# Optimization experiments

Hardware: AMD Instinct MI355X
Metric: run time of the kernel (lower is better)

Reference implementation:

```python
import jax, jax.numpy as jnp
import numpy as np
from functools import partial

EPS = 1e-5
SCALE = 2
NUM_BLOCKS = 2


def _layernorm(x, g, b):
    mu = jnp.mean(x, axis=-1, keepdims=True)
    var = jnp.var(x, axis=-1, keepdims=True)
    return (x - mu) * jax.lax.rsqrt(var + EPS) * g + b


def _rwkv(tokens, td, Wk, Wv, Wr, Wo, ln_g, ln_b):
    # tokens: (B, N, C)
    x = _layernorm(tokens, ln_g, ln_b)
    k = jnp.einsum('bnc,oc->bno', x, Wk)
    v = jnp.einsum('bnc,oc->bno', x, Wv)
    r = jax.nn.sigmoid(jnp.einsum('bnc,oc->bno', x, Wr))
    decay = jnp.exp(-jax.nn.relu(td))  # (C,)

    def step(state, inp):
        kt, vt, rt = inp  # each (B, C)
        state = state * decay + kt
        return state, rt * (state + vt)

    B, N, C = tokens.shape
    init = jnp.zeros((B, C), dtype=tokens.dtype)
    # scan over token axis
    _, yT = jax.lax.scan(step, init, (k.transpose(1, 0, 2), v.transpose(1, 0, 2), r.transpose(1, 0, 2)))
    y = yT.transpose(1, 0, 2)  # (B, N, C)
    return jnp.einsum('bnc,oc->bno', y, Wo)


def reference(x, global_state, cond_gw, cond_gb, cond_bw, cond_bb,
              td, Wk, Wv, Wr, Wo, ln_g, ln_b, gp_w, gp_b, bp_w, bp_b):
    B, C, H, W = x.shape
    Hp, Wp = H * SCALE, W * SCALE
    # bilinear upsample, half-pixel centers == torch align_corners=False
    x_up = jax.image.resize(x, (B, C, Hp, Wp), method='bilinear')
    tokens = x_up.reshape(B, C, Hp * Wp).transpose(0, 2, 1)  # (B, N, C)
    # semantic conditioning (FiLM from global state)
    gamma = (global_state @ cond_gw.T + cond_gb)[:, None, :]
    beta = (global_state @ cond_bw.T + cond_bb)[:, None, :]
    tokens = tokens * (1.0 + gamma) + beta

    out = x_up
    cur = tokens
    for i in range(NUM_BLOCKS):
        if i > 0:
            cur = out.reshape(B, C, Hp * Wp).transpose(0, 2, 1)
        t = _rwkv(cur, td[i], Wk[i], Wv[i], Wr[i], Wo[i], ln_g[i], ln_b[i])
        g = jnp.einsum('bnc,oc->bno', t, gp_w[i]) + gp_b[i]
        bt = jnp.einsum('bnc,oc->bno', t, bp_w[i]) + bp_b[i]
        g = g.transpose(0, 2, 1).reshape(B, C, Hp, Wp)
        bt = bt.transpose(0, 2, 1).reshape(B, C, Hp, Wp)
        out = out * (1.0 + jnp.tanh(g)) + bt
    return out


def setup_inputs() -> dict:
    key = jax.random.key(0)
    ks = jax.random.split(key, 16)
    B, C, H, W = 8, 128, 64, 64
    w_scale = 0.02
    inp = {
        'x': jax.random.normal(ks[0], (B, C, H, W), jnp.float32),
        'global_state': jax.random.normal(ks[1], (B, C), jnp.float32),
        'cond_gw': jax.random.normal(ks[2], (C, C), jnp.float32) * w_scale,
        'cond_gb': jnp.zeros((C,), jnp.float32),
        'cond_bw': jax.random.normal(ks[3], (C, C), jnp.float32) * w_scale,
        'cond_bb': jnp.zeros((C,), jnp.float32),
        'td': jax.random.uniform(ks[4], (NUM_BLOCKS, C), jnp.float32),
        'Wk': jax.random.normal(ks[5], (NUM_BLOCKS, C, C), jnp.float32) * w_scale,
        'Wv': jax.random.normal(ks[6], (NUM_BLOCKS, C, C), jnp.float32) * w_scale,
        'Wr': jax.random.normal(ks[7], (NUM_BLOCKS, C, C), jnp.float32) * w_scale,
        'Wo': jax.random.normal(ks[8], (NUM_BLOCKS, C, C), jnp.float32) * w_scale,
        'ln_g': jnp.ones((NUM_BLOCKS, C), jnp.float32),
        'ln_b': jnp.zeros((NUM_BLOCKS, C), jnp.float32),
        'gp_w': jax.random.normal(ks[9], (NUM_BLOCKS, C, C), jnp.float32) * w_scale,
        'gp_b': jnp.zeros((NUM_BLOCKS, C), jnp.float32),
        'bp_w': jax.random.normal(ks[10], (NUM_BLOCKS, C, C), jnp.float32) * w_scale,
        'bp_b': jnp.zeros((NUM_BLOCKS, C), jnp.float32),
    }
    return inp
```

## Files before the change

kernel.cpp:

```cpp
#include <hip/hip_runtime.h>
#include <hip/hip_bf16.h>

#define BB 8
#define CC 128
#define NN 16384
#define MM (BB * NN)
#define NCH 128
#define CLN 128

typedef __attribute__((ext_vector_type(8))) short short8;
typedef __attribute__((ext_vector_type(4))) float floatx4;
typedef unsigned short u16;
typedef unsigned int u32;

__device__ __forceinline__ float bf2f(u16 h) {
  u32 u = ((u32)h) << 16;
  return __builtin_bit_cast(float, u);
}
__device__ __forceinline__ u16 f2bf(float f) {
  u32 u = __builtin_bit_cast(u32, f);
  u32 r = u + 0x7FFFu + ((u >> 16) & 1u);
  return (u16)(r >> 16);
}

__global__ void film_kernel(const float* __restrict__ gs, const float* __restrict__ gw,
                            const float* __restrict__ gb, const float* __restrict__ bw,
                            const float* __restrict__ bb, float* __restrict__ gamma,
                            float* __restrict__ beta) {
  int idx = blockIdx.x * 256 + threadIdx.x;
  int b = idx >> 7, c = idx & 127;
  float sg = 0.f, sb = 0.f;
  for (int j = 0; j < 128; ++j) {
    float g = gs[b * 128 + j];
    sg += g * gw[c * 128 + j];
    sb += g * bw[c * 128 + j];
  }
  gamma[idx] = sg + gb[c];
  beta[idx] = sb + bb[c];
}

__global__ void convert_kernel(const float* __restrict__ Wk, const float* __restrict__ Wv,
                               const float* __restrict__ Wr, const float* __restrict__ Wo,
                               const float* __restrict__ gp, const float* __restrict__ bp,
                               u16* __restrict__ dst) {
  int idx = blockIdx.x * 256 + threadIdx.x;
  int which = idx >> 15;
  int off = idx & 32767;
  const float* s;
  switch (which) {
    case 0: s = Wk; break; case 1: s = Wv; break; case 2: s = Wr; break;
    case 3: s = Wo; break; case 4: s = gp; break; default: s = bp; break;
  }
  dst[idx] = f2bf(s[off]);
}

template <int UPS>
__global__ __launch_bounds__(256) void prep_kernel(
    const float* __restrict__ src, const float* __restrict__ gamma,
    const float* __restrict__ beta, const float* __restrict__ lng,
    const float* __restrict__ lnb, float* __restrict__ outp, u16* __restrict__ xn) {
  __shared__ float tile[64][129];
  __shared__ float smu[64], srs[64];
  int bidx = blockIdx.x;
  int half = bidx & 1;
  int ho = (bidx >> 1) & 127;
  int b = bidx >> 8;
  int wo0 = half * 64;
  int tid = threadIdx.x;
  int tk = tid & 63;
  int wo = wo0 + tk;
  int c0 = tid >> 6;
  int j0 = 0, j1 = 0, i0 = 0, i1 = 0;
  float wy0 = 0.f, wy1 = 0.f, wx0 = 0.f, wx1 = 0.f;
  if (UPS) {
    int jj = ho >> 1;
    if ((ho & 1) == 0) { j0 = jj > 0 ? jj - 1 : 0; j1 = jj; wy0 = 0.25f; wy1 = 0.75f; }
    else               { j0 = jj; j1 = jj < 63 ? jj + 1 : 63; wy0 = 0.75f; wy1 = 0.25f; }
    int ii = wo >> 1;
    if ((wo & 1) == 0) { i0 = ii > 0 ? ii - 1 : 0; i1 = ii; wx0 = 0.25f; wx1 = 0.75f; }
    else               { i0 = ii; i1 = ii < 63 ? ii + 1 : 63; wx0 = 0.75f; wx1 = 0.25f; }
  }
  for (int it = 0; it < 32; ++it) {
    int c = it * 4 + c0;
    float v;
    if (UPS) {
      const float* xp = src + ((size_t)(b * 128 + c)) * 4096;
      v = wy0 * (wx0 * xp[j0 * 64 + i0] + wx1 * xp[j0 * 64 + i1]) +
          wy1 * (wx0 * xp[j1 * 64 + i0] + wx1 * xp[j1 * 64 + i1]);
      outp[((size_t)(b * 128 + c)) * 16384 + ho * 128 + wo] = v;
      v = v * (1.f + gamma[b * 128 + c]) + beta[b * 128 + c];
    } else {
      v = src[((size_t)(b * 128 + c)) * 16384 + ho * 128 + wo];
    }
    tile[tk][c] = v;
  }
  __syncthreads();
  {
    int token = tid >> 2, q = tid & 3;
    float s = 0.f, s2 = 0.f;
    for (int j = 0; j < 32; ++j) { float v = tile[token][q * 32 + j]; s += v; s2 += v * v; }
    s += __shfl_xor(s, 1); s2 += __shfl_xor(s2, 1);
    s += __shfl_xor(s, 2); s2 += __shfl_xor(s2, 2);
    if (q == 0) {
      float mu = s * 0.0078125f;
      float var = s2 * 0.0078125f - mu * mu;
      smu[token] = mu;
      srs[token] = rsqrtf(var + 1e-5f);
    }
  }
  __syncthreads();
  size_t base = ((size_t)b * 16384 + ho * 128 + wo0) * 128;
  for (int it = 0; it < 32; ++it) {
    int idx = it * 256 + tid;
    int token = idx >> 7, c = idx & 127;
    float v = (tile[token][c] - smu[token]) * srs[token] * lng[c] + lnb[c];
    xn[base + idx] = f2bf(v);
  }
}

__global__ __launch_bounds__(256, 2) void gemm_y_kernel(
    const u16* __restrict__ A, const u16* __restrict__ Wv_, const u16* __restrict__ Wr_,
    const u16* __restrict__ Wk_, const float* __restrict__ td,
    u16* __restrict__ outY, u16* __restrict__ outRD, float* __restrict__ Sbuf) {
  __shared__ u16 Alds[128 * 128];
  __shared__ u16 Wlds[128 * 128];
  __shared__ float SWT[512];
  int tid = threadIdx.x;
  int wave = tid >> 6, lane = tid & 63;
  int l15 = lane & 15, l4 = lane >> 4;
  size_t row0 = (size_t)blockIdx.x * 128;

#pragma unroll
  for (int it = 0; it < 8; ++it) {
    int idx = it * 256 + tid;
    int rr = idx >> 4, s = idx & 15;
    uint4 d = *(const uint4*)(A + (row0 + rr) * 128 + s * 8);
    *(uint4*)(&Alds[rr * 128 + ((s ^ (rr & 15)) << 3)]) = d;
  }
#pragma unroll
  for (int it = 0; it < 8; ++it) {
    int idx = it * 256 + tid;
    int rr = idx >> 4, s = idx & 15;
    uint4 d = *(const uint4*)(Wv_ + rr * 128 + s * 8);
    *(uint4*)(&Wlds[rr * 128 + ((s ^ (rr & 15)) << 3)]) = d;
  }
  float av[8], dd[8], d4a[8];
#pragma unroll
  for (int ni = 0; ni < 8; ++ni) {
    float a = fmaxf(td[ni * 16 + l15], 0.f);
    av[ni] = a;
    float d = __expf(-a);
    dd[ni] = d;
    float d2 = d * d;
    d4a[ni] = d2 * d2;
  }
  __syncthreads();

  floatx4 accv[2][8];
#pragma unroll
  for (int mi = 0; mi < 2; ++mi)
#pragma unroll
    for (int ni = 0; ni < 8; ++ni) accv[mi][ni] = (floatx4){0.f, 0.f, 0.f, 0.f};
#pragma unroll
  for (int kk = 0; kk < 4; ++kk) {
    int seg = kk * 4 + l4;
    short8 a0 = *(const short8*)(&Alds[(wave * 32 + l15) * 128 + ((seg ^ l15) << 3)]);
    short8 a1 = *(const short8*)(&Alds[(wave * 32 + 16 + l15) * 128 + ((seg ^ l15) << 3)]);
#pragma unroll
    for (int ni = 0; ni < 8; ++ni) {
      short8 bfr = *(const short8*)(&Wlds[(ni * 16 + l15) * 128 + ((seg ^ l15) << 3)]);
      accv[0][ni] = __builtin_amdgcn_mfma_f32_16x16x32_bf16(a0, bfr, accv[0][ni], 0, 0, 0);
      accv[1][ni] = __builtin_amdgcn_mfma_f32_16x16x32_bf16(a1, bfr, accv[1][ni], 0, 0, 0);
    }
  }
  __syncthreads();
#pragma unroll
  for (int it = 0; it < 8; ++it) {
    int idx = it * 256 + tid;
    int rr = idx >> 4, s = idx & 15;
    uint4 d = *(const uint4*)(Wr_ + rr * 128 + s * 8);
    *(uint4*)(&Wlds[rr * 128 + ((s ^ (rr & 15)) << 3)]) = d;
  }
  __syncthreads();
  floatx4 accr[2][8];
#pragma unroll
  for (int mi = 0; mi < 2; ++mi)
#pragma unroll
    for (int ni = 0; ni < 8; ++ni) accr[mi][ni] = (floatx4){0.f, 0.f, 0.f, 0.f};
#pragma unroll
  for (int kk = 0; kk < 4; ++kk) {
    int seg = kk * 4 + l4;
    short8 a0 = *(const short8*)(&Alds[(wave * 32 + l15) * 128 + ((seg ^ l15) << 3)]);
    short8 a1 = *(const short8*)(&Alds[(wave * 32 + 16 + l15) * 128 + ((seg ^ l15) << 3)]);
#pragma unroll
    for (int ni = 0; ni < 8; ++ni) {
      short8 bfr = *(const short8*)(&Wlds[(ni * 16 + l15) * 128 + ((seg ^ l15) << 3)]);
      accr[0][ni] = __builtin_amdgcn_mfma_f32_16x16x32_bf16(a0, bfr, accr[0][ni], 0, 0, 0);
      accr[1][ni] = __builtin_amdgcn_mfma_f32_16x16x32_bf16(a1, bfr, accr[1][ni], 0, 0, 0);
    }
  }
  u32 rvp[2][8][2], rp[2][8][2];
#pragma unroll
  for (int mi = 0; mi < 2; ++mi) {
#pragma unroll
    for (int ni = 0; ni < 8; ++ni) {
      int c = ni * 16 + l15;
      int T0 = wave * 32 + mi * 16 + l4 * 4;
      float w = __expf(-av[ni] * (float)(T0 + 1));
      float rs[4], rv[4];
#pragma unroll
      for (int j = 0; j < 4; ++j) {
        float sg = 1.f / (1.f + __expf(-accr[mi][ni][j]));
        rs[j] = sg;
        rv[j] = sg * accv[mi][ni][j];
        outRD[(row0 + T0 + j) * 128 + c] = f2bf(sg * w);
        w *= dd[ni];
      }
      rvp[mi][ni][0] = (u32)f2bf(rv[0]) | ((u32)f2bf(rv[1]) << 16);
      rvp[mi][ni][1] = (u32)f2bf(rv[2]) | ((u32)f2bf(rv[3]) << 16);
      rp[mi][ni][0] = (u32)f2bf(rs[0]) | ((u32)f2bf(rs[1]) << 16);
      rp[mi][ni][1] = (u32)f2bf(rs[2]) | ((u32)f2bf(rs[3]) << 16);
    }
  }
  __syncthreads();
#pragma unroll
  for (int it = 0; it < 8; ++it) {
    int idx = it * 256 + tid;
    int rr = idx >> 4, s = idx & 15;
    uint4 d = *(const uint4*)(Wk_ + rr * 128 + s * 8);
    *(uint4*)(&Wlds[rr * 128 + ((s ^ (rr & 15)) << 3)]) = d;
  }
  __syncthreads();
  floatx4 acck[2][8];
#pragma unroll
  for (int mi = 0; mi < 2; ++mi)
#pragma unroll
    for (int ni = 0; ni < 8; ++ni) acck[mi][ni] = (floatx4){0.f, 0.f, 0.f, 0.f};
#pragma unroll
  for (int kk = 0; kk < 4; ++kk) {
    int seg = kk * 4 + l4;
    short8 a0 = *(const short8*)(&Alds[(wave * 32 + l15) * 128 + ((seg ^ l15) << 3)]);
    short8 a1 = *(const short8*)(&Alds[(wave * 32 + 16 + l15) * 128 + ((seg ^ l15) << 3)]);
#pragma unroll
    for (int ni = 0; ni < 8; ++ni) {
      short8 bfr = *(const short8*)(&Wlds[(ni * 16 + l15) * 128 + ((seg ^ l15) << 3)]);
      acck[0][ni] = __builtin_amdgcn_mfma_f32_16x16x32_bf16(a0, bfr, acck[0][ni], 0, 0, 0);
      acck[1][ni] = __builtin_amdgcn_mfma_f32_16x16x32_bf16(a1, bfr, acck[1][ni], 0, 0, 0);
    }
  }
  float Elr[2][8];
  float B0r[8];
#pragma unroll
  for (int ni = 0; ni < 8; ++ni) {
    float d = dd[ni], d4 = d4a[ni];
    float d8 = d4 * d4, d16 = d8 * d8;
    float I[2];
#pragma unroll
    for (int mi = 0; mi < 2; ++mi) {
      float p0 = acck[mi][ni][0];
      float p1 = d * p0 + acck[mi][ni][1];
      float p2 = d * p1 + acck[mi][ni][2];
      float p3 = d * p2 + acck[mi][ni][3];
      acck[mi][ni][0] = p0; acck[mi][ni][1] = p1;
      acck[mi][ni][2] = p2; acck[mi][ni][3] = p3;
      float Iv = p3;
      float t1 = __shfl_up(Iv, 16);
      if (l4 >= 1) Iv += d4 * t1;
      float t2 = __shfl_up(Iv, 32);
      if (l4 >= 2) Iv += d8 * t2;
      float ex = __shfl_up(Iv, 16);
      Elr[mi][ni] = (l4 == 0) ? 0.f : ex;
      I[mi] = Iv;
    }
    float B0 = __shfl(I[0], 48 + l15);
    float B1 = __shfl(I[1], 48 + l15);
    B0r[ni] = B0;
    if (l4 == 0) SWT[wave * 128 + ni * 16 + l15] = B1 + d16 * B0;
  }
  __syncthreads();
  u16* YW = Wlds;
#pragma unroll
  for (int ni = 0; ni < 8; ++ni) {
    int c = ni * 16 + l15;
    float d = dd[ni], d4 = d4a[ni];
    float d8 = d4 * d4, d12 = d8 * d4, d16 = d8 * d8, d32 = d16 * d16;
    float e = 0.f;
#pragma unroll
    for (int wv = 0; wv < 3; ++wv)
      if (wv < wave) e = e * d32 + SWT[wv * 128 + c];
    float d4l = (l4 == 0) ? 1.f : ((l4 == 1) ? d4 : ((l4 == 2) ? d8 : d12));
#pragma unroll
    for (int mi = 0; mi < 2; ++mi) {
      float Emi = (mi == 0) ? e : (e * d16 + B0r[ni]);
      float Sb = Elr[mi][ni] + d4l * Emi;
      float w = d;
#pragma unroll
      for (int j = 0; j < 4; ++j) {
        float s = acck[mi][ni][j] + w * Sb;
        w *= d;
        float rvv = bf2f((u16)(rvp[mi][ni][j >> 1] >> ((j & 1) * 16)));
        float rss = bf2f((u16)(rp[mi][ni][j >> 1] >> ((j & 1) * 16)));
        float y = rvv + rss * s;
        int row = wave * 32 + mi * 16 + l4 * 4 + j;
        int colsw = c ^ (((row >> 2) & 3) << 4);
        YW[row * 128 + colsw] = f2bf(y);
      }
    }
  }
  if (tid < 128) {
    float a = fmaxf(td[tid], 0.f);
    float d32 = __expf(-32.f * a);
    float e = 0.f;
#pragma unroll
    for (int wv = 0; wv < 4; ++wv) e = e * d32 + SWT[wv * 128 + tid];
    Sbuf[(blockIdx.x & 127) * 1024 + (blockIdx.x >> 7) * 128 + tid] = e;
  }
  __syncthreads();
#pragma unroll
  for (int it = 0; it < 8; ++it) {
    int idx = it * 256 + tid;
    int row = idx >> 4, cb = (idx & 15) * 8;
    int csw = cb ^ (((row >> 2) & 3) << 4);
    uint4 dv = *(const uint4*)(&YW[row * 128 + csw]);
    *(uint4*)(outY + (row0 + row) * 128 + cb) = dv;
  }
}

__global__ __launch_bounds__(256) void scan2_kernel(const float* __restrict__ S,
                                                    const float* __restrict__ td,
                                                    float* __restrict__ init) {
  int wave = threadIdx.x >> 6, lane = threadIdx.x & 63;
  int bc = blockIdx.x * 4 + wave;
  int c = bc & 127;
  float a1 = __expf(-fmaxf(td[c], 0.f) * 128.f);
  float s0 = S[(2 * lane) * 1024 + bc];
  float s1 = S[(2 * lane + 1) * 1024 + bc];
  float s = s1 + a1 * s0;
  float a = a1 * a1;
  for (int off = 1; off < 64; off <<= 1) {
    float ss = __shfl_up(s, off);
    float aa = __shfl_up(a, off);
    if (lane >= off) { s = s + a * ss; a = a * aa; }
  }
  float e = __shfl_up(s, 1);
  if (lane == 0) e = 0.f;
  init[(2 * lane) * 1024 + bc] = e;
  init[(2 * lane + 1) * 1024 + bc] = a1 * e + s0;
}

__global__ __launch_bounds__(512, 4) void tail_kernel(
    const u16* __restrict__ yl, const u16* __restrict__ rd,
    const float* __restrict__ init,
    const u16* __restrict__ Wo, const u16* __restrict__ Wg, const u16* __restrict__ Wb,
    const float* __restrict__ gpb, const float* __restrict__ bpb,
    float* __restrict__ outp) {
  __shared__ u32 SMEM[8192];
  __shared__ float IL[128];
  u16* Y = (u16*)SMEM;
  u16* T2 = (u16*)SMEM;
  u32* MB = SMEM;

  int tid = threadIdx.x;
  int wave = tid >> 6, lane = tid & 63;
  int l15 = lane & 15, l4 = lane >> 4;
  int b = blockIdx.x >> 7;
  int chunk = blockIdx.x & 127;
  size_t ebase = ((size_t)b * 16384 + (size_t)chunk * 128) * 128;

  if (tid < 128) IL[tid] = init[chunk * 1024 + b * 128 + tid];
  __syncthreads();

#pragma unroll
  for (int it = 0; it < 4; ++it) {
    int idx = it * 512 + tid;
    int t = idx >> 4;
    int c8 = (idx & 15) * 8;
    uint4 yv = *(const uint4*)(yl + ebase + (size_t)t * 128 + c8);
    uint4 rv = *(const uint4*)(rd + ebase + (size_t)t * 128 + c8);
    u32 o[4];
    u32 yq[4] = {yv.x, yv.y, yv.z, yv.w};
    u32 rq[4] = {rv.x, rv.y, rv.z, rv.w};
#pragma unroll
    for (int q = 0; q < 4; ++q) {
      float y0 = bf2f((u16)(yq[q] & 0xffff)) + bf2f((u16)(rq[q] & 0xffff)) * IL[c8 + 2 * q];
      float y1 = bf2f((u16)(yq[q] >> 16)) + bf2f((u16)(rq[q] >> 16)) * IL[c8 + 2 * q + 1];
      o[q] = (u32)f2bf(y0) | ((u32)f2bf(y1) << 16);
    }
    uint4 ov = {o[0], o[1], o[2], o[3]};
    *(uint4*)(&Y[t * 128 + (((c8 >> 3) ^ (t & 15)) << 3)]) = ov;
  }
  __syncthreads();

  int ob = wave * 16;
  short8 wof[4];
#pragma unroll
  for (int kk = 0; kk < 4; ++kk)
    wof[kk] = *(const short8*)(Wo + (ob + l15) * 128 + kk * 32 + l4 * 8);
  floatx4 acc[8];
#pragma unroll
  for (int ni = 0; ni < 8; ++ni) acc[ni] = (floatx4){0.f, 0.f, 0.f, 0.f};
#pragma unroll
  for (int kk = 0; kk < 4; ++kk) {
    int seg = kk * 4 + l4;
#pragma unroll
    for (int ni = 0; ni < 8; ++ni) {
      short8 yf = *(const short8*)(&Y[(ni * 16 + l15) * 128 + ((seg ^ l15) << 3)]);
      acc[ni] = __builtin_amdgcn_mfma_f32_16x16x32_bf16(wof[kk], yf, acc[ni], 0, 0, 0);
    }
  }
  __syncthreads();

#pragma unroll
  for (int ni = 0; ni < 8; ++ni) {
    int tok = ni * 16 + l15;
#pragma unroll
    for (int j = 0; j < 4; j += 2) {
      int o = ob + l4 * 4 + j;
      u32 pack = (u32)f2bf(acc[ni][j]) | ((u32)f2bf(acc[ni][j + 1]) << 16);
      int pos = tok * 128 + ((((o >> 3) ^ (tok & 15)) << 3) | (o & 7));
      *(u32*)(T2 + pos) = pack;
    }
  }
  __syncthreads();

  short8 wgf[4], wbf2[4];
#pragma unroll
  for (int kk = 0; kk < 4; ++kk) {
    wgf[kk]  = *(const short8*)(Wg + (ob + l15) * 128 + kk * 32 + l4 * 8);
    wbf2[kk] = *(const short8*)(Wb + (ob + l15) * 128 + kk * 32 + l4 * 8);
  }
  floatx4 ag[8], ab[8];
#pragma unroll
  for (int ni = 0; ni < 8; ++ni) {
    ag[ni] = (floatx4){0.f, 0.f, 0.f, 0.f};
    ab[ni] = (floatx4){0.f, 0.f, 0.f, 0.f};
  }
#pragma unroll
  for (int kk = 0; kk < 4; ++kk) {
    int seg = kk * 4 + l4;
#pragma unroll
    for (int ni = 0; ni < 8; ++ni) {
      short8 tf = *(const short8*)(&T2[(ni * 16 + l15) * 128 + ((seg ^ l15) << 3)]);
      ag[ni] = __builtin_amdgcn_mfma_f32_16x16x32_bf16(wgf[kk], tf, ag[ni], 0, 0, 0);
      ab[ni] = __builtin_amdgcn_mfma_f32_16x16x32_bf16(wbf2[kk], tf, ab[ni], 0, 0, 0);
    }
  }
  __syncthreads();

#pragma unroll
  for (int h = 0; h < 2; ++h) {
    if ((wave >> 2) == h) {
      int orel0 = (wave & 3) * 16;
#pragma unroll
      for (int ni = 0; ni < 8; ++ni) {
        int tok = ni * 16 + l15;
#pragma unroll
        for (int j = 0; j < 4; ++j) {
          int orel = orel0 + l4 * 4 + j;
          int o = h * 64 + orel;
          float g = ag[ni][j] + gpb[o];
          float t1 = __expf(2.f * g);
          float m = 2.f - 2.f / (t1 + 1.f);
          float bt = ab[ni][j] + bpb[o];
          int rot = ((orel & 3) << 2) | ((orel >> 2) & 3);
          MB[orel * 128 + ((((tok >> 3) ^ rot) << 3) | (tok & 7))] =
              (u32)f2bf(m) | ((u32)f2bf(bt) << 16);
        }
      }
    }
    __syncthreads();
#pragma unroll
    for (int it = 0; it < 2; ++it) {
      int idx = it * 512 + tid;
      int orel = idx >> 4, seg = idx & 15;
      int o = h * 64 + orel;
      int rot = ((orel & 3) << 2) | ((orel >> 2) & 3);
      int sp = ((seg ^ rot) << 3);
      uint4 mb0 = *(const uint4*)(&MB[orel * 128 + sp]);
      uint4 mb1 = *(const uint4*)(&MB[orel * 128 + sp + 4]);
      float* op = outp + ((size_t)(b * 128 + o)) * 16384 + chunk * 128 + seg * 8;
      float4 o0 = *(float4*)op;
      float4 o1 = *(float4*)(op + 4);
      o0.x = o0.x * bf2f((u16)(mb0.x & 0xffff)) + bf2f((u16)(mb0.x >> 16));
      o0.y = o0.y * bf2f((u16)(mb0.y & 0xffff)) + bf2f((u16)(mb0.y >> 16));
      o0.z = o0.z * bf2f((u16)(mb0.z & 0xffff)) + bf2f((u16)(mb0.z >> 16));
      o0.w = o0.w * bf2f((u16)(mb0.w & 0xffff)) + bf2f((u16)(mb0.w >> 16));
      o1.x = o1.x * bf2f((u16)(mb1.x & 0xffff)) + bf2f((u16)(mb1.x >> 16));
      o1.y = o1.y * bf2f((u16)(mb1.y & 0xffff)) + bf2f((u16)(mb1.y >> 16));
      o1.z = o1.z * bf2f((u16)(mb1.z & 0xffff)) + bf2f((u16)(mb1.z >> 16));
      o1.w = o1.w * bf2f((u16)(mb1.w & 0xffff)) + bf2f((u16)(mb1.w >> 16));
      *(float4*)op = o0;
      *(float4*)(op + 4) = o1;
    }
    __syncthreads();
  }
}

extern "C" void kernel_launch(void* const* d_in, const int* in_sizes, int n_in,
                              void* d_out, int out_size, void* d_ws, size_t ws_size,
                              hipStream_t stream) {
  const float* x        = (const float*)d_in[0];
  const float* gs       = (const float*)d_in[1];
  const float* cond_gw  = (const float*)d_in[2];
  const float* cond_gb  = (const float*)d_in[3];
  const float* cond_bw  = (const float*)d_in[4];
  const float* cond_bb  = (const float*)d_in[5];
  const float* td       = (const float*)d_in[6];
  const float* Wk       = (const float*)d_in[7];
  const float* Wv       = (const float*)d_in[8];
  const float* Wr       = (const float*)d_in[9];
  const float* Wo       = (const float*)d_in[10];
  const float* ln_g     = (const float*)d_in[11];
  const float* ln_b     = (const float*)d_in[12];
  const float* gp_w     = (const float*)d_in[13];
  const float* gp_b     = (const float*)d_in[14];
  const float* bp_w     = (const float*)d_in[15];
  const float* bp_b     = (const float*)d_in[16];
  float* outp = (float*)d_out;

  char* w = (char*)d_ws;
  float* gamma = (float*)w; w += 4096;
  float* beta  = (float*)w; w += 4096;
  u16* wbf     = (u16*)w;   w += 6 * 2 * 16384 * sizeof(u16);
  u16* xn      = (u16*)w;   w += (size_t)MM * 128 * sizeof(u16);
  u16* ybuf    = (u16*)w;   w += (size_t)MM * 128 * sizeof(u16);
  u16* rdbuf   = (u16*)w;   w += (size_t)MM * 128 * sizeof(u16);
  float* Sbuf  = (float*)w; w += NCH * 1024 * sizeof(float);
  float* ibuf  = (float*)w; w += NCH * 1024 * sizeof(float);

  film_kernel<<<4, 256, 0, stream>>>(gs, cond_gw, cond_gb, cond_bw, cond_bb, gamma, beta);
  convert_kernel<<<768, 256, 0, stream>>>(Wk, Wv, Wr, Wo, gp_w, bp_w, wbf);

  for (int blk = 0; blk < 2; ++blk) {
    const u16* bWk = wbf + 0 * 32768 + blk * 16384;
    const u16* bWv = wbf + 1 * 32768 + blk * 16384;
    const u16* bWr = wbf + 2 * 32768 + blk * 16384;
    const u16* bWo = wbf + 3 * 32768 + blk * 16384;
    const u16* bGp = wbf + 4 * 32768 + blk * 16384;
    const u16* bBp = wbf + 5 * 32768 + blk * 16384;
    const float* tdi = td + blk * 128;

    if (blk == 0)
      prep_kernel<1><<<2048, 256, 0, stream>>>(x, gamma, beta, ln_g, ln_b, outp, xn);
    else
      prep_kernel<0><<<2048, 256, 0, stream>>>(outp, nullptr, nullptr, ln_g + 128,
                                               ln_b + 128, nullptr, xn);

    gemm_y_kernel<<<1024, 256, 0, stream>>>(xn, bWv, bWr, bWk, tdi, ybuf, rdbuf, Sbuf);
    scan2_kernel<<<256, 256, 0, stream>>>(Sbuf, tdi, ibuf);
    tail_kernel<<<1024, 512, 0, stream>>>(ybuf, rdbuf, ibuf, bWo, bGp, bBp,
                                          gp_b + blk * 128, bp_b + blk * 128, outp);
  }
}
```

Measured before the change: 268.9 us.

## Compute chunk states in separate pass to drop intermediate rd buffer

```diff
diff --git a/kernel.cpp b/kernel.cpp
--- a/kernel.cpp
+++ b/kernel.cpp
@@ -118,18 +118,16 @@
   }
 }
 
-__global__ __launch_bounds__(256, 2) void gemm_y_kernel(
-    const u16* __restrict__ A, const u16* __restrict__ Wv_, const u16* __restrict__ Wr_,
-    const u16* __restrict__ Wk_, const float* __restrict__ td,
-    u16* __restrict__ outY, u16* __restrict__ outRD, float* __restrict__ Sbuf) {
+__global__ __launch_bounds__(256) void gemm_S_kernel(
+    const u16* __restrict__ A, const u16* __restrict__ W0,
+    const float* __restrict__ td, float* __restrict__ Sbuf) {
   __shared__ u16 Alds[128 * 128];
   __shared__ u16 Wlds[128 * 128];
-  __shared__ float SWT[512];
+  __shared__ float Sred[512];
   int tid = threadIdx.x;
   int wave = tid >> 6, lane = tid & 63;
   int l15 = lane & 15, l4 = lane >> 4;
   size_t row0 = (size_t)blockIdx.x * 128;
-
 #pragma unroll
   for (int it = 0; it < 8; ++it) {
     int idx = it * 256 + tid;
@@ -141,14 +139,111 @@
   for (int it = 0; it < 8; ++it) {
     int idx = it * 256 + tid;
     int rr = idx >> 4, s = idx & 15;
+    uint4 d = *(const uint4*)(W0 + rr * 128 + s * 8);
+    *(uint4*)(&Wlds[rr * 128 + ((s ^ (rr & 15)) << 3)]) = d;
+  }
+  __syncthreads();
+  floatx4 acc[2][8];
+#pragma unroll
+  for (int mi = 0; mi < 2; ++mi)
+#pragma unroll
+    for (int ni = 0; ni < 8; ++ni) acc[mi][ni] = (floatx4){0.f, 0.f, 0.f, 0.f};
+#pragma unroll
+  for (int kk = 0; kk < 4; ++kk) {
+    int seg = kk * 4 + l4;
+    short8 a0 = *(const short8*)(&Alds[(wave * 32 + l15) * 128 + ((seg ^ l15) << 3)]);
+    short8 a1 = *(const short8*)(&Alds[(wave * 32 + 16 + l15) * 128 + ((seg ^ l15) << 3)]);
+#pragma unroll
+    for (int ni = 0; ni < 8; ++ni) {
+      short8 bfr = *(const short8*)(&Wlds[(ni * 16 + l15) * 128 + ((seg ^ l15) << 3)]);
+      acc[0][ni] = __builtin_amdgcn_mfma_f32_16x16x32_bf16(a0, bfr, acc[0][ni], 0, 0, 0);
+      acc[1][ni] = __builtin_amdgcn_mfma_f32_16x16x32_bf16(a1, bfr, acc[1][ni], 0, 0, 0);
+    }
+  }
+  int T0 = wave * 32 + l4 * 4;
+#pragma unroll
+  for (int ni = 0; ni < 8; ++ni) {
+    int c = ni * 16 + l15;
+    float a = fmaxf(td[c], 0.f);
+    float E = __expf(-a * (float)(127 - T0));
+    float r1 = __expf(a);
+    float r16 = __expf(a * 16.f);
+    float w = E, sum;
+    sum  = w * acc[0][ni][0]; w *= r1;
+    sum += w * acc[0][ni][1]; w *= r1;
+    sum += w * acc[0][ni][2]; w *= r1;
+    sum += w * acc[0][ni][3];
+    w = E * r16;
+    sum += w * acc[1][ni][0]; w *= r1;
+    sum += w * acc[1][ni][1]; w *= r1;
+    sum += w * acc[1][ni][2]; w *= r1;
+    sum += w * acc[1][ni][3];
+    sum += __shfl_xor(sum, 16);
+    sum += __shfl_xor(sum, 32);
+    if (l4 == 0) Sred[wave * 128 + c] = sum;
+  }
+  __syncthreads();
+  if (tid < 128) {
+    float s = Sred[tid] + Sred[128 + tid] + Sred[256 + tid] + Sred[384 + tid];
+    Sbuf[(blockIdx.x & 127) * 1024 + (blockIdx.x >> 7) * 128 + tid] = s;
+  }
+}
+
+__global__ __launch_bounds__(256) void scan2_kernel(const float* __restrict__ S,
+                                                    const float* __restrict__ td,
+                                                    float* __restrict__ init) {
+  int wave = threadIdx.x >> 6, lane = threadIdx.x & 63;
+  int bc = blockIdx.x * 4 + wave;
+  int c = bc & 127;
+  float a1 = __expf(-fmaxf(td[c], 0.f) * 128.f);
+  float s0 = S[(2 * lane) * 1024 + bc];
+  float s1 = S[(2 * lane + 1) * 1024 + bc];
+  float s = s1 + a1 * s0;
+  float a = a1 * a1;
+  for (int off = 1; off < 64; off <<= 1) {
+    float ss = __shfl_up(s, off);
+    float aa = __shfl_up(a, off);
+    if (lane >= off) { s = s + a * ss; a = a * aa; }
+  }
+  float e = __shfl_up(s, 1);
+  if (lane == 0) e = 0.f;
+  init[(2 * lane) * 1024 + bc] = e;
+  init[(2 * lane + 1) * 1024 + bc] = a1 * e + s0;
+}
+
+__global__ __launch_bounds__(256, 2) void gemm_y_kernel(
+    const u16* __restrict__ A, const u16* __restrict__ Wv_, const u16* __restrict__ Wr_,
+    const u16* __restrict__ Wk_, const float* __restrict__ td,
+    const float* __restrict__ init_, u16* __restrict__ outY) {
+  __shared__ u16 Alds[128 * 128];
+  __shared__ u16 Wlds[128 * 128];
+  __shared__ float SWT[512];
+  __shared__ float ILS[128];
+  int tid = threadIdx.x;
+  int wave = tid >> 6, lane = tid & 63;
+  int l15 = lane & 15, l4 = lane >> 4;
+  size_t row0 = (size_t)blockIdx.x * 128;
+  int bI = blockIdx.x >> 7, chunkI = blockIdx.x & 127;
+  if (tid < 128) ILS[tid] = init_[chunkI * 1024 + bI * 128 + tid];
+
+#pragma unroll
+  for (int it = 0; it < 8; ++it) {
+    int idx = it * 256 + tid;
+    int rr = idx >> 4, s = idx & 15;
+    uint4 d = *(const uint4*)(A + (row0 + rr) * 128 + s * 8);
+    *(uint4*)(&Alds[rr * 128 + ((s ^ (rr & 15)) << 3)]) = d;
+  }
+#pragma unroll
+  for (int it = 0; it < 8; ++it) {
+    int idx = it * 256 + tid;
+    int rr = idx >> 4, s = idx & 15;
     uint4 d = *(const uint4*)(Wv_ + rr * 128 + s * 8);
     *(uint4*)(&Wlds[rr * 128 + ((s ^ (rr & 15)) << 3)]) = d;
   }
-  float av[8], dd[8], d4a[8];
+  float dd[8], d4a[8];
 #pragma unroll
   for (int ni = 0; ni < 8; ++ni) {
     float a = fmaxf(td[ni * 16 + l15], 0.f);
-    av[ni] = a;
     float d = __expf(-a);
     dd[ni] = d;
     float d2 = d * d;
@@ -204,17 +299,12 @@
   for (int mi = 0; mi < 2; ++mi) {
 #pragma unroll
     for (int ni = 0; ni < 8; ++ni) {
-      int c = ni * 16 + l15;
-      int T0 = wave * 32 + mi * 16 + l4 * 4;
-      float w = __expf(-av[ni] * (float)(T0 + 1));
       float rs[4], rv[4];
 #pragma unroll
       for (int j = 0; j < 4; ++j) {
         float sg = 1.f / (1.f + __expf(-accr[mi][ni][j]));
         rs[j] = sg;
         rv[j] = sg * accv[mi][ni][j];
-        outRD[(row0 + T0 + j) * 128 + c] = f2bf(sg * w);
-        w *= dd[ni];
       }
       rvp[mi][ni][0] = (u32)f2bf(rv[0]) | ((u32)f2bf(rv[1]) << 16);
       rvp[mi][ni][1] = (u32)f2bf(rv[2]) | ((u32)f2bf(rv[3]) << 16);
@@ -284,7 +374,7 @@
     int c = ni * 16 + l15;
     float d = dd[ni], d4 = d4a[ni];
     float d8 = d4 * d4, d12 = d8 * d4, d16 = d8 * d8, d32 = d16 * d16;
-    float e = 0.f;
+    float e = ILS[c];
 #pragma unroll
     for (int wv = 0; wv < 3; ++wv)
       if (wv < wave) e = e * d32 + SWT[wv * 128 + c];
@@ -307,14 +397,6 @@
       }
     }
   }
-  if (tid < 128) {
-    float a = fmaxf(td[tid], 0.f);
-    float d32 = __expf(-32.f * a);
-    float e = 0.f;
-#pragma unroll
-    for (int wv = 0; wv < 4; ++wv) e = e * d32 + SWT[wv * 128 + tid];
-    Sbuf[(blockIdx.x & 127) * 1024 + (blockIdx.x >> 7) * 128 + tid] = e;
-  }
   __syncthreads();
 #pragma unroll
   for (int it = 0; it < 8; ++it) {
@@ -326,36 +408,12 @@
   }
 }
 
-__global__ __launch_bounds__(256) void scan2_kernel(const float* __restrict__ S,
-                                                    const float* __restrict__ td,
-                                                    float* __restrict__ init) {
-  int wave = threadIdx.x >> 6, lane = threadIdx.x & 63;
-  int bc = blockIdx.x * 4 + wave;
-  int c = bc & 127;
-  float a1 = __expf(-fmaxf(td[c], 0.f) * 128.f);
-  float s0 = S[(2 * lane) * 1024 + bc];
-  float s1 = S[(2 * lane + 1) * 1024 + bc];
-  float s = s1 + a1 * s0;
-  float a = a1 * a1;
-  for (int off = 1; off < 64; off <<= 1) {
-    float ss = __shfl_up(s, off);
-    float aa = __shfl_up(a, off);
-    if (lane >= off) { s = s + a * ss; a = a * aa; }
-  }
-  float e = __shfl_up(s, 1);
-  if (lane == 0) e = 0.f;
-  init[(2 * lane) * 1024 + bc] = e;
-  init[(2 * lane + 1) * 1024 + bc] = a1 * e + s0;
-}
-
 __global__ __launch_bounds__(512, 4) void tail_kernel(
-    const u16* __restrict__ yl, const u16* __restrict__ rd,
-    const float* __restrict__ init,
+    const u16* __restrict__ yl,
     const u16* __restrict__ Wo, const u16* __restrict__ Wg, const u16* __restrict__ Wb,
     const float* __restrict__ gpb, const float* __restrict__ bpb,
     float* __restrict__ outp) {
   __shared__ u32 SMEM[8192];
-  __shared__ float IL[128];
   u16* Y = (u16*)SMEM;
   u16* T2 = (u16*)SMEM;
   u32* MB = SMEM;
@@ -367,27 +425,13 @@
   int chunk = blockIdx.x & 127;
   size_t ebase = ((size_t)b * 16384 + (size_t)chunk * 128) * 128;
 
-  if (tid < 128) IL[tid] = init[chunk * 1024 + b * 128 + tid];
-  __syncthreads();
-
 #pragma unroll
   for (int it = 0; it < 4; ++it) {
     int idx = it * 512 + tid;
     int t = idx >> 4;
     int c8 = (idx & 15) * 8;
     uint4 yv = *(const uint4*)(yl + ebase + (size_t)t * 128 + c8);
-    uint4 rv = *(const uint4*)(rd + ebase + (size_t)t * 128 + c8);
-    u32 o[4];
-    u32 yq[4] = {yv.x, yv.y, yv.z, yv.w};
-    u32 rq[4] = {rv.x, rv.y, rv.z, rv.w};
-#pragma unroll
-    for (int q = 0; q < 4; ++q) {
-      float y0 = bf2f((u16)(yq[q] & 0xffff)) + bf2f((u16)(rq[q] & 0xffff)) * IL[c8 + 2 * q];
-      float y1 = bf2f((u16)(yq[q] >> 16)) + bf2f((u16)(rq[q] >> 16)) * IL[c8 + 2 * q + 1];
-      o[q] = (u32)f2bf(y0) | ((u32)f2bf(y1) << 16);
-    }
-    uint4 ov = {o[0], o[1], o[2], o[3]};
-    *(uint4*)(&Y[t * 128 + (((c8 >> 3) ^ (t & 15)) << 3)]) = ov;
+    *(uint4*)(&Y[t * 128 + (((c8 >> 3) ^ (t & 15)) << 3)]) = yv;
   }
   __syncthreads();
 
@@ -524,7 +568,6 @@
   u16* wbf     = (u16*)w;   w += 6 * 2 * 16384 * sizeof(u16);
   u16* xn      = (u16*)w;   w += (size_t)MM * 128 * sizeof(u16);
   u16* ybuf    = (u16*)w;   w += (size_t)MM * 128 * sizeof(u16);
-  u16* rdbuf   = (u16*)w;   w += (size_t)MM * 128 * sizeof(u16);
   float* Sbuf  = (float*)w; w += NCH * 1024 * sizeof(float);
   float* ibuf  = (float*)w; w += NCH * 1024 * sizeof(float);
 
@@ -546,9 +589,10 @@
       prep_kernel<0><<<2048, 256, 0, stream>>>(outp, nullptr, nullptr, ln_g + 128,
                                                ln_b + 128, nullptr, xn);
 
-    gemm_y_kernel<<<1024, 256, 0, stream>>>(xn, bWv, bWr, bWk, tdi, ybuf, rdbuf, Sbuf);
+    gemm_S_kernel<<<1024, 256, 0, stream>>>(xn, bWk, tdi, Sbuf);
     scan2_kernel<<<256, 256, 0, stream>>>(Sbuf, tdi, ibuf);
-    tail_kernel<<<1024, 512, 0, stream>>>(ybuf, rdbuf, ibuf, bWo, bGp, bBp,
+    gemm_y_kernel<<<1024, 256, 0, stream>>>(xn, bWv, bWr, bWk, tdi, ibuf, ybuf);
+    tail_kernel<<<1024, 512, 0, stream>>>(ybuf, bWo, bGp, bBp,
                                           gp_b + blk * 128, bp_b + blk * 128, outp);
   }
 }
```

New measurement: 277.1 us. 3.1% more time.
